# Optimization experiments

Hardware: AMD Instinct MI355X
Metric: run time of the kernel (lower is better)

## Reference

```python
import jax, jax.numpy as jnp
import numpy as np

N, E = 50000, 800000
IN_DIM, HID, OUT = 128, 64, 64
NEG_SLOPE = 0.2  # PyG GATConv default leaky_relu slope


def glorot(key, shape):
    fan_in, fan_out = shape[0], shape[-1]
    lim = jnp.sqrt(6.0 / (fan_in + fan_out))
    return jax.random.uniform(key, shape, minval=-lim, maxval=lim, dtype=jnp.float32)


def setup_inputs() -> dict:
    key = jax.random.key(0)
    ks = jax.random.split(key, 10)
    x = jax.random.normal(ks[0], (N, IN_DIM), dtype=jnp.float32)
    edge_index = jax.random.randint(ks[1], (2, E), 0, N, dtype=jnp.int64)
    # GATConv layer 1: heads=2, concat=False
    W1 = glorot(ks[2], (IN_DIM, 2 * HID))
    att_src1 = glorot(ks[3], (1, 2, HID))[0]   # [2, HID]
    att_dst1 = glorot(ks[4], (1, 2, HID))[0]
    b1 = jnp.zeros((HID,), jnp.float32)
    # GATConv layer 2: heads=1, concat=False
    W2 = glorot(ks[5], (HID, OUT))
    att_src2 = glorot(ks[6], (1, 1, OUT))[0]   # [1, OUT]
    att_dst2 = glorot(ks[7], (1, 1, OUT))[0]
    b2 = jnp.zeros((OUT,), jnp.float32)
    return {"x": x, "edge_index": edge_index, "W1": W1, "att_src1": att_src1,
            "att_dst1": att_dst1, "b1": b1, "W2": W2, "att_src2": att_src2,
            "att_dst2": att_dst2, "b2": b2}


def gat_conv(x, src, dst, W, att_src, att_dst, bias, heads, out_ch):
    n = x.shape[0]
    h = (x @ W).reshape(n, heads, out_ch)              # [N,H,C]
    a_src = jnp.einsum('nhc,hc->nh', h, att_src)       # [N,H]
    a_dst = jnp.einsum('nhc,hc->nh', h, att_dst)
    e = jax.nn.leaky_relu(a_src[src] + a_dst[dst], NEG_SLOPE)  # [E,H]
    # softmax over incoming edges per destination node (stable)
    e_max = jax.ops.segment_max(e, dst, num_segments=n)
    ex = jnp.exp(e - e_max[dst])
    denom = jax.ops.segment_sum(ex, dst, num_segments=n)
    alpha = ex / (denom[dst] + 1e-16)                  # [E,H]
    msg = h[src] * alpha[:, :, None]                   # [E,H,C]
    out = jax.ops.segment_sum(msg, dst, num_segments=n)
    return out.mean(axis=1) + bias                     # concat=False -> head mean


def reference(x, edge_index, W1, att_src1, att_dst1, b1, W2, att_src2, att_dst2, b2):
    n = x.shape[0]
    loop = jnp.arange(n, dtype=edge_index.dtype)
    src = jnp.concatenate([edge_index[0], loop])       # PyG add_self_loops
    dst = jnp.concatenate([edge_index[1], loop])
    x1 = gat_conv(x, src, dst, W1, att_src1, att_dst1, b1, 2, HID)
    x1 = jax.nn.elu(x1)
    # eval mode: dropedge and dropout are identity
    out = gat_conv(x1, src, dst, W2, att_src2, att_dst2, b2, 1, OUT)
    return out
```

## Files before the change

### kernel.cpp

```cpp
#include <hip/hip_runtime.h>
#include <math.h>

#define IN_DIM 128
#define HID 64
#define NEG_SLOPE 0.2f
#define CHUNK 4096
#define GCAP 6144

typedef __attribute__((ext_vector_type(8))) short bf16x8;
typedef __attribute__((ext_vector_type(4))) float f32x4;
typedef __attribute__((ext_vector_type(2))) float v2f;

__device__ __forceinline__ float wmax(float v){
  #pragma unroll
  for (int o = 32; o > 0; o >>= 1) v = fmaxf(v, __shfl_xor(v, o));
  return v;
}
__device__ __forceinline__ float wsum(float v){
  #pragma unroll
  for (int o = 32; o > 0; o >>= 1) v += __shfl_xor(v, o);
  return v;
}
__device__ __forceinline__ unsigned short f2bf(float f){
  union { float f; unsigned u; } v; v.f = f;
  unsigned r = v.u + 0x7fffu + ((v.u >> 16) & 1u);
  return (unsigned short)(r >> 16);
}
__device__ __forceinline__ float bl(unsigned u){
  union { unsigned u; float f; } v; v.u = u << 16; return v.f;
}
__device__ __forceinline__ float bh(unsigned u){
  union { unsigned u; float f; } v; v.u = u & 0xffff0000u; return v.f;
}
__device__ __forceinline__ v2f up2(unsigned u){
  v2f r; r[0] = bl(u); r[1] = bh(u); return r;
}

__device__ __forceinline__ void incl_scan256(int* sh, int tid){
  #pragma unroll
  for (int off = 1; off < 256; off <<= 1){
    int v = sh[tid];
    if (tid >= off) v += sh[tid - off];
    __syncthreads();
    sh[tid] = v;
    __syncthreads();
  }
}


__global__ __launch_bounds__(256) void prep(const int* __restrict__ ei, int E, int NBLK,
                                            unsigned* __restrict__ packed,
                                            int* __restrict__ binCnt,
                                            const float* __restrict__ W1,
                                            const float* __restrict__ W2,
                                            unsigned short* __restrict__ W1t,
                                            unsigned short* __restrict__ W2t,
                                            int* __restrict__ row_ptr, int N){
  int tid = threadIdx.x;
  if ((int)blockIdx.x < NBLK){
    __shared__ int lh[256];
    lh[tid] = 0; __syncthreads();
    int base = blockIdx.x * CHUNK;
    #pragma unroll
    for (int j = 0; j < CHUNK / 256; j++){
      int e = base + j * 256 + tid;
      if (e < E){
        unsigned s = (unsigned)ei[e];
        unsigned d = (unsigned)ei[E + e];
        packed[e] = (d << 16) | s;
        atomicAdd(&lh[d >> 8], 1);
      }
    }
    __syncthreads();
    if (lh[tid] > 0) atomicAdd(&binCnt[tid], lh[tid]);
  } else {
    int t = (blockIdx.x - NBLK) * 256 + tid;
    if (t < 128 * 128){
      int n = t >> 7, k = t & 127;
      W1t[n * 128 + k] = f2bf(W1[k * 128 + n]);
    }
    int t2 = t - 128 * 128;
    if (t2 >= 0 && t2 < 64 * 64){
      int n = t2 >> 6, k = t2 & 63;
      W2t[n * 64 + k] = f2bf(W2[k * 64 + n]);
    }
    if (t == 0) row_ptr[N] = E;
  }
}

__global__ __launch_bounds__(256) void scatter_bins(const unsigned* __restrict__ packed, int E,
                                                    const int* __restrict__ binCnt,
                                                    int* __restrict__ binOff,
                                                    unsigned* __restrict__ binned){
  __shared__ int bc[256], lh[256], lbase[256], gpos[256], lcur[256];
  __shared__ unsigned buf[CHUNK];
  int tid = threadIdx.x;
  int cg = binCnt[tid];
  bc[tid] = cg;
  lh[tid] = 0;
  __syncthreads();
  incl_scan256(bc, tid);
  int binBase_t = bc[tid] - cg;
  int base = blockIdx.x * CHUNK;
  int rem = E - base;
  unsigned v[CHUNK / 256];
  #pragma unroll
  for (int j = 0; j < CHUNK / 256; j++){
    int i = j * 256 + tid;
    if (i < rem){ v[j] = packed[base + i]; atomicAdd(&lh[v[j] >> 24], 1); }
  }
  __syncthreads();
  lbase[tid] = lh[tid]; __syncthreads();
  incl_scan256(lbase, tid);
  int myExcl = tid ? lbase[tid - 1] : 0;
  __syncthreads();
  lbase[tid] = myExcl;
  lcur[tid] = myExcl;
  if (lh[tid] > 0) gpos[tid] = binBase_t + atomicAdd(&binOff[tid], lh[tid]);
  __syncthreads();
  #pragma unroll
  for (int j = 0; j < CHUNK / 256; j++){
    int i = j * 256 + tid;
    if (i < rem){
      int b = v[j] >> 24;
      int p = atomicAdd(&lcur[b], 1);
      buf[p] = v[j];
    }
  }
  __syncthreads();
  int cn = rem < CHUNK ? rem : CHUNK;
  for (int i = tid; i < cn; i += 256){
    unsigned u = buf[i];
    int b = u >> 24;
    binned[gpos[b] + (i - lbase[b])] = u;
  }
}

__global__ __launch_bounds__(256) void group_sort(const unsigned* __restrict__ binned,
                                                  const int* __restrict__ binCnt,
                                                  unsigned* __restrict__ sorted,
                                                  int* __restrict__ row_ptr, int N){
  __shared__ unsigned A[GCAP], B[GCAP];
  __shared__ int sc[256], h2[256], rs[256], cur[256];
  int g = blockIdx.x, tid = threadIdx.x;
  int cg = binCnt[tid];
  sc[tid] = cg;
  h2[tid] = 0;
  __syncthreads();
  incl_scan256(sc, tid);
  int base = sc[g] - binCnt[g];
  int cnt = binCnt[g]; if (cnt > GCAP) cnt = GCAP;
  __syncthreads();
  for (int i = tid; i < cnt; i += 256){
    unsigned u = binned[base + i];
    A[i] = u;
    atomicAdd(&h2[(u >> 16) & 255], 1);
  }
  __syncthreads();
  rs[tid] = h2[tid]; __syncthreads();
  incl_scan256(rs, tid);
  int excl = tid ? rs[tid - 1] : 0;
  __syncthreads();
  rs[tid] = excl; cur[tid] = excl;
  int d = g * 256 + tid;
  if (d < N) row_ptr[d] = base + excl;
  __syncthreads();
  for (int i = tid; i < cnt; i += 256){
    unsigned u = A[i];
    int p = atomicAdd(&cur[(u >> 16) & 255], 1);
    B[p] = u;
  }
  __syncthreads();
  for (int i = tid; i < cnt; i += 256)
    sorted[base + i] = B[i];
}


template<int K, int NC, int HEADS>
__global__ __launch_bounds__(512) void gemm_mfma(const float* __restrict__ X,
    const unsigned short* __restrict__ Wt, const float* __restrict__ asrc,
    const float* __restrict__ adst, unsigned short* __restrict__ Hb,
    float* __restrict__ aa, int n_rows)
{
  constexpr int MT = 128;
  constexpr int KP = K + 8;
  constexpr int CP = NC + 4;
  constexpr int MF = MT / 16;
  constexpr int NFt = NC / 16;
  constexpr int WPN = 8 / NFt;
  constexpr int MFW = MF / WPN;
  constexpr unsigned SM1 = (unsigned)(MT + NC) * KP * 2;
  constexpr unsigned SM2 = (unsigned)MT * CP * 4;
  __shared__ char smem[SM1 > SM2 ? SM1 : SM2];
  unsigned short* xa = (unsigned short*)smem;
  unsigned short* wl = xa + MT * KP;
  int tid = threadIdx.x;
  int n0 = blockIdx.x * MT;

  for (int idx = tid; idx < MT * (K / 4); idx += 512){
    int n = idx / (K / 4), k4 = idx % (K / 4);
    float4 v = make_float4(0.f, 0.f, 0.f, 0.f);
    if (n0 + n < n_rows) v = *(const float4*)&X[(size_t)(n0 + n) * K + k4 * 4];
    ushort4 pk; pk.x = f2bf(v.x); pk.y = f2bf(v.y); pk.z = f2bf(v.z); pk.w = f2bf(v.w);
    *(ushort4*)&xa[n * KP + k4 * 4] = pk;
  }
  for (int idx = tid; idx < NC * (K / 8); idx += 512){
    int n = idx / (K / 8), k8 = idx % (K / 8);
    uint4 v = *(const uint4*)&Wt[(size_t)n * K + k8 * 8];
    *(uint4*)&wl[n * KP + k8 * 8] = v;
  }
  __syncthreads();

  int lane = tid & 63, w = tid >> 6;
  int m = lane & 15, q = lane >> 4;
  int nf = w % NFt;
  int mseg = w / NFt;
  f32x4 acc[MFW];
  #pragma unroll
  for (int i = 0; i < MFW; i++)
    #pragma unroll
    for (int r = 0; r < 4; r++) acc[i][r] = 0.f;

  #pragma unroll
  for (int ks = 0; ks < K / 32; ks++){
    bf16x8 bg = *(const bf16x8*)&wl[(nf * 16 + m) * KP + ks * 32 + q * 8];
    #pragma unroll
    for (int i = 0; i < MFW; i++){
      bf16x8 af = *(const bf16x8*)&xa[((mseg * MFW + i) * 16 + m) * KP + ks * 32 + q * 8];
      acc[i] = __builtin_amdgcn_mfma_f32_16x16x32_bf16(af, bg, acc[i], 0, 0, 0);
    }
  }
  __syncthreads();
  float* C = (float*)smem;
  #pragma unroll
  for (int i = 0; i < MFW; i++)
    #pragma unroll
    for (int r = 0; r < 4; r++)
      C[((mseg * MFW + i) * 16 + q * 4 + r) * CP + nf * 16 + m] = acc[i][r];
  __syncthreads();

  constexpr int CH = NC / 4;
  int row = tid >> 2;
  int c0 = (tid & 3) * CH;
  int n = n0 + row;
  int head = (HEADS == 2) ? (c0 >> 6) : 0;
  float s_p = 0.f, d_p = 0.f;
  unsigned short hb[CH];
  #pragma unroll
  for (int c = 0; c < CH; c += 4){
    f32x4 v = *(const f32x4*)&C[row * CP + c0 + c];
    #pragma unroll
    for (int u = 0; u < 4; u++){
      int ch = (c0 + c + u) & 63;
      s_p += v[u] * asrc[head * 64 + ch];
      d_p += v[u] * adst[head * 64 + ch];
      hb[c + u] = f2bf(v[u]);
    }
  }
  if (n < n_rows){
    #pragma unroll
    for (int c = 0; c < CH; c += 8){
      uint4 pk;
      pk.x = (unsigned)hb[c]     | ((unsigned)hb[c + 1] << 16);
      pk.y = (unsigned)hb[c + 2] | ((unsigned)hb[c + 3] << 16);
      pk.z = (unsigned)hb[c + 4] | ((unsigned)hb[c + 5] << 16);
      pk.w = (unsigned)hb[c + 6] | ((unsigned)hb[c + 7] << 16);
      *(uint4*)&Hb[(size_t)n * NC + c0 + c] = pk;
    }
  }
  s_p += __shfl_xor(s_p, 1);
  d_p += __shfl_xor(d_p, 1);
  if (HEADS == 2){
    if ((tid & 1) == 0 && n < n_rows){
      aa[(size_t)n * 4 + head]     = s_p;
      aa[(size_t)n * 4 + 2 + head] = d_p;
    }
  } else {
    s_p += __shfl_xor(s_p, 2);
    d_p += __shfl_xor(d_p, 2);
    if ((tid & 3) == 0 && n < n_rows){
      aa[(size_t)n * 2]     = s_p;
      aa[(size_t)n * 2 + 1] = d_p;
    }
  }
}


__global__ void agg_layer1(const int* __restrict__ row_ptr, const unsigned* __restrict__ sorted,
                           const float* __restrict__ aa, const unsigned short* __restrict__ h1b,
                           const float* __restrict__ b1, float* __restrict__ x1, int n_nodes){
  int d = (blockIdx.x * blockDim.x + threadIdx.x) >> 6;
  int lane = threadIdx.x & 63;
  if (d >= n_nodes) return;
  int rp0 = row_ptr[d];
  int deg = row_ptr[d + 1] - rp0;
  float2 adv = *(const float2*)&aa[d * 4 + 2];
  int s = -1;
  if (lane < deg) s = (int)(sorted[rp0 + lane] & 0xffffu);
  else if (lane == deg) s = d;
  float e0 = -INFINITY, e1 = -INFINITY;
  if (s >= 0){
    float2 asv = *(const float2*)&aa[s * 4];
    float t0 = asv.x + adv.x;
    float t1 = asv.y + adv.y;
    e0 = t0 >= 0.f ? t0 : NEG_SLOPE * t0;
    e1 = t1 >= 0.f ? t1 : NEG_SLOPE * t1;
  }
  float m0 = wmax(e0), m1 = wmax(e1);
  float p0 = (s >= 0) ? __expf(e0 - m0) : 0.f;
  float p1 = (s >= 0) ? __expf(e1 - m1) : 0.f;
  float al0 = p0 / (wsum(p0) + 1e-16f);
  float al1 = p1 / (wsum(p1) + 1e-16f);
  int ne = deg + 1;
  int g = lane >> 4, c = lane & 15;
  v2f acc[4] = {{0.f,0.f},{0.f,0.f},{0.f,0.f},{0.f,0.f}};
  #pragma unroll 2
  for (int j0 = 0; j0 < ne; j0 += 4){
    int j = j0 + g;
    int sj = __shfl(s, j);
    float a0 = __shfl(al0, j);
    float a1 = __shfl(al1, j);
    if (j < ne){
      uint4 v = ((const uint4*)(h1b + (size_t)sj * 128))[c];
      float a = (c < 8) ? a0 : a1;
      v2f av = {a, a};
      acc[0] = av * up2(v.x) + acc[0];
      acc[1] = av * up2(v.y) + acc[1];
      acc[2] = av * up2(v.z) + acc[2];
      acc[3] = av * up2(v.w) + acc[3];
    }
  }
  float accf[8] = {acc[0][0], acc[0][1], acc[1][0], acc[1][1],
                   acc[2][0], acc[2][1], acc[3][0], acc[3][1]};
  #pragma unroll
  for (int i = 0; i < 8; i++){
    accf[i] += __shfl_xor(accf[i], 16);
    accf[i] += __shfl_xor(accf[i], 32);
  }
  float outv[8];
  #pragma unroll
  for (int i = 0; i < 8; i++){
    float o = __shfl_xor(accf[i], 8);
    outv[i] = 0.5f * (accf[i] + o);
  }
  if (g == 0 && c < 8){
    float r[8];
    #pragma unroll
    for (int i = 0; i < 8; i++){
      float v = outv[i] + b1[c * 8 + i];
      r[i] = v > 0.f ? v : expm1f(v);
    }
    float* p = &x1[(size_t)d * 64 + c * 8];
    *(float4*)p       = make_float4(r[0], r[1], r[2], r[3]);
    *(float4*)(p + 4) = make_float4(r[4], r[5], r[6], r[7]);
  }
}

__global__ void agg_layer2(const int* __restrict__ row_ptr, const unsigned* __restrict__ sorted,
                           const float* __restrict__ aa, const unsigned short* __restrict__ h2b,
                           const float* __restrict__ b2, float* __restrict__ out, int n_nodes){
  int d = (blockIdx.x * blockDim.x + threadIdx.x) >> 6;
  int lane = threadIdx.x & 63;
  if (d >= n_nodes) return;
  int rp0 = row_ptr[d];
  int deg = row_ptr[d + 1] - rp0;
  float ad = aa[d * 2 + 1];
  int s = -1;
  if (lane < deg) s = (int)(sorted[rp0 + lane] & 0xffffu);
  else if (lane == deg) s = d;
  float e = -INFINITY;
  if (s >= 0){
    float t = aa[s * 2 + 0] + ad;
    e = t >= 0.f ? t : NEG_SLOPE * t;
  }
  float m = wmax(e);
  float p = (s >= 0) ? __expf(e - m) : 0.f;
  float al = p / (wsum(p) + 1e-16f);
  int ne = deg + 1;
  int g = lane >> 3, c = lane & 7;
  v2f acc[4] = {{0.f,0.f},{0.f,0.f},{0.f,0.f},{0.f,0.f}};
  #pragma unroll 2
  for (int j0 = 0; j0 < ne; j0 += 8){
    int j = j0 + g;
    int sj = __shfl(s, j);
    float a = __shfl(al, j);
    if (j < ne){
      uint4 v = ((const uint4*)(h2b + (size_t)sj * 64))[c];
      v2f av = {a, a};
      acc[0] = av * up2(v.x) + acc[0];
      acc[1] = av * up2(v.y) + acc[1];
      acc[2] = av * up2(v.z) + acc[2];
      acc[3] = av * up2(v.w) + acc[3];
    }
  }
  float accf[8] = {acc[0][0], acc[0][1], acc[1][0], acc[1][1],
                   acc[2][0], acc[2][1], acc[3][0], acc[3][1]};
  #pragma unroll
  for (int i = 0; i < 8; i++){
    accf[i] += __shfl_xor(accf[i], 8);
    accf[i] += __shfl_xor(accf[i], 16);
    accf[i] += __shfl_xor(accf[i], 32);
  }
  if (lane < 8){
    float r[8];
    #pragma unroll
    for (int i = 0; i < 8; i++) r[i] = accf[i] + b2[lane * 8 + i];
    float* q = &out[(size_t)d * 64 + lane * 8];
    *(float4*)q       = make_float4(r[0], r[1], r[2], r[3]);
    *(float4*)(q + 4) = make_float4(r[4], r[5], r[6], r[7]);
  }
}

extern "C" void kernel_launch(void* const* d_in, const int* in_sizes, int n_in,
                              void* d_out, int out_size, void* d_ws, size_t ws_size,
                              hipStream_t stream){
  const float* x     = (const float*)d_in[0];
  const int*   ei    = (const int*)d_in[1];
  const float* W1    = (const float*)d_in[2];
  const float* asrc1 = (const float*)d_in[3];
  const float* adst1 = (const float*)d_in[4];
  const float* b1    = (const float*)d_in[5];
  const float* W2    = (const float*)d_in[6];
  const float* asrc2 = (const float*)d_in[7];
  const float* adst2 = (const float*)d_in[8];
  const float* b2    = (const float*)d_in[9];
  float* out = (float*)d_out;
  int N = in_sizes[0] / IN_DIM;
  int E = in_sizes[1] / 2;
  int NG = (N + 255) >> 8;
  int NBLK = (E + CHUNK - 1) / CHUNK;
  int ngrp = (N + 3) / 4;

  char* p = (char*)d_ws;
  unsigned short* h1b = (unsigned short*)p;  p += (size_t)N * 128 * 2;
  unsigned short* h2b = (unsigned short*)p;  p += (size_t)N * 64 * 2;
  float* x1  = (float*)p;                    p += (size_t)N * 64 * 4;
  float* aa1 = (float*)p;                    p += (size_t)N * 4 * 4;
  float* aa2 = (float*)p;                    p += (size_t)N * 2 * 4;
  unsigned* packed = (unsigned*)p;           p += (size_t)E * 4;
  unsigned* binned = (unsigned*)p;           p += (size_t)E * 4;
  unsigned* sorted = (unsigned*)p;           p += (size_t)E * 4;
  int* row_ptr   = (int*)p;                  p += (size_t)(N + 1) * 4;
  int* binCnt    = (int*)p;                  p += 256 * 4;
  int* binOff    = (int*)p;                  p += 256 * 4;
  unsigned short* W1t = (unsigned short*)p;  p += 128 * 128 * 2;
  unsigned short* W2t = (unsigned short*)p;

  hipMemsetAsync(binCnt, 0, 512 * sizeof(int), stream);
  prep<<<NBLK + 80, 256, 0, stream>>>(ei, E, NBLK, packed, binCnt,
                                      W1, W2, W1t, W2t, row_ptr, N);
  scatter_bins<<<NBLK, 256, 0, stream>>>(packed, E, binCnt, binOff, binned);
  group_sort<<<NG, 256, 0, stream>>>(binned, binCnt, sorted, row_ptr, N);
  gemm_mfma<128, 128, 2><<<(N + 127) / 128, 512, 0, stream>>>(
      x, W1t, asrc1, adst1, h1b, aa1, N);
  agg_layer1<<<ngrp, 256, 0, stream>>>(row_ptr, sorted, aa1, h1b, b1, x1, N);
  gemm_mfma<64, 64, 1><<<(N + 127) / 128, 512, 0, stream>>>(
      x1, W2t, asrc2, adst2, h2b, aa2, N);
  agg_layer2<<<ngrp, 256, 0, stream>>>(row_ptr, sorted, aa2, h2b, b2, out, N);
}
```

Before: 235.9 us.

## Fuse layer-1 aggregation with layer-2 GEMM via per-block bf16 MFMA tile

Layer-1 aggregation and the layer-2 linear transform now run in one kernel. Each 64-thread block aggregates 16 destination nodes in sequence, writes the ELU outputs as bf16 into shared memory, then runs a 16x64x64 MFMA against W2t and writes h2b and the attention scalars directly. This removes the fp32 x1 round trip through global memory and one kernel launch. In exchange each wave handles its 16 nodes serially, block-level parallelism is lower, and x1 is now rounded to bf16 before the GEMM.

```diff
diff --git a/kernel.cpp b/kernel.cpp
--- a/kernel.cpp
+++ b/kernel.cpp
@@ -285,76 +285,137 @@
   }
 }
 
-
-__global__ void agg_layer1(const int* __restrict__ row_ptr, const unsigned* __restrict__ sorted,
-                           const float* __restrict__ aa, const unsigned short* __restrict__ h1b,
-                           const float* __restrict__ b1, float* __restrict__ x1, int n_nodes){
-  int d = (blockIdx.x * blockDim.x + threadIdx.x) >> 6;
-  int lane = threadIdx.x & 63;
-  if (d >= n_nodes) return;
-  int rp0 = row_ptr[d];
-  int deg = row_ptr[d + 1] - rp0;
-  float2 adv = *(const float2*)&aa[d * 4 + 2];
-  int s = -1;
-  if (lane < deg) s = (int)(sorted[rp0 + lane] & 0xffffu);
-  else if (lane == deg) s = d;
-  float e0 = -INFINITY, e1 = -INFINITY;
-  if (s >= 0){
-    float2 asv = *(const float2*)&aa[s * 4];
-    float t0 = asv.x + adv.x;
-    float t1 = asv.y + adv.y;
-    e0 = t0 >= 0.f ? t0 : NEG_SLOPE * t0;
-    e1 = t1 >= 0.f ? t1 : NEG_SLOPE * t1;
-  }
-  float m0 = wmax(e0), m1 = wmax(e1);
-  float p0 = (s >= 0) ? __expf(e0 - m0) : 0.f;
-  float p1 = (s >= 0) ? __expf(e1 - m1) : 0.f;
-  float al0 = p0 / (wsum(p0) + 1e-16f);
-  float al1 = p1 / (wsum(p1) + 1e-16f);
-  int ne = deg + 1;
+__global__ __launch_bounds__(64) void agg1_gemm2(const int* __restrict__ row_ptr,
+    const unsigned* __restrict__ sorted, const float* __restrict__ aa,
+    const unsigned short* __restrict__ h1b, const float* __restrict__ b1,
+    const unsigned short* __restrict__ W2t, const float* __restrict__ asrc2,
+    const float* __restrict__ adst2, unsigned short* __restrict__ h2b,
+    float* __restrict__ aa2, int n_nodes)
+{
+  __shared__ unsigned short xt[16 * 72];
+  __shared__ float Cl[16 * 68];
+  int lane = threadIdx.x;
+  int d0 = blockIdx.x * 16;
+
   int g = lane >> 4, c = lane & 15;
-  v2f acc[4] = {{0.f,0.f},{0.f,0.f},{0.f,0.f},{0.f,0.f}};
-  #pragma unroll 2
-  for (int j0 = 0; j0 < ne; j0 += 4){
-    int j = j0 + g;
-    int sj = __shfl(s, j);
-    float a0 = __shfl(al0, j);
-    float a1 = __shfl(al1, j);
-    if (j < ne){
-      uint4 v = ((const uint4*)(h1b + (size_t)sj * 128))[c];
-      float a = (c < 8) ? a0 : a1;
-      v2f av = {a, a};
-      acc[0] = av * up2(v.x) + acc[0];
-      acc[1] = av * up2(v.y) + acc[1];
-      acc[2] = av * up2(v.z) + acc[2];
-      acc[3] = av * up2(v.w) + acc[3];
-    }
-  }
-  float accf[8] = {acc[0][0], acc[0][1], acc[1][0], acc[1][1],
-                   acc[2][0], acc[2][1], acc[3][0], acc[3][1]};
-  #pragma unroll
-  for (int i = 0; i < 8; i++){
-    accf[i] += __shfl_xor(accf[i], 16);
-    accf[i] += __shfl_xor(accf[i], 32);
-  }
-  float outv[8];
-  #pragma unroll
-  for (int i = 0; i < 8; i++){
-    float o = __shfl_xor(accf[i], 8);
-    outv[i] = 0.5f * (accf[i] + o);
-  }
-  if (g == 0 && c < 8){
-    float r[8];
+  for (int jd = 0; jd < 16; jd++){
+    int d = d0 + jd;
+    if (d >= n_nodes) break;
+    int rp0 = row_ptr[d];
+    int deg = row_ptr[d + 1] - rp0;
+    float2 adv = *(const float2*)&aa[d * 4 + 2];
+    int s = -1;
+    if (lane < deg) s = (int)(sorted[rp0 + lane] & 0xffffu);
+    else if (lane == deg) s = d;
+    float e0 = -INFINITY, e1 = -INFINITY;
+    if (s >= 0){
+      float2 asv = *(const float2*)&aa[s * 4];
+      float t0 = asv.x + adv.x;
+      float t1 = asv.y + adv.y;
+      e0 = t0 >= 0.f ? t0 : NEG_SLOPE * t0;
+      e1 = t1 >= 0.f ? t1 : NEG_SLOPE * t1;
+    }
+    float m0 = wmax(e0), m1 = wmax(e1);
+    float p0 = (s >= 0) ? __expf(e0 - m0) : 0.f;
+    float p1 = (s >= 0) ? __expf(e1 - m1) : 0.f;
+    float al0 = p0 / (wsum(p0) + 1e-16f);
+    float al1 = p1 / (wsum(p1) + 1e-16f);
+    int ne = deg + 1;
+    v2f acc[4] = {{0.f,0.f},{0.f,0.f},{0.f,0.f},{0.f,0.f}};
+    #pragma unroll 2
+    for (int j0 = 0; j0 < ne; j0 += 4){
+      int j = j0 + g;
+      int sj = __shfl(s, j);
+      float a0 = __shfl(al0, j);
+      float a1 = __shfl(al1, j);
+      if (j < ne){
+        uint4 v = ((const uint4*)(h1b + (size_t)sj * 128))[c];
+        float a = (c < 8) ? a0 : a1;
+        v2f av = {a, a};
+        acc[0] = av * up2(v.x) + acc[0];
+        acc[1] = av * up2(v.y) + acc[1];
+        acc[2] = av * up2(v.z) + acc[2];
+        acc[3] = av * up2(v.w) + acc[3];
+      }
+    }
+    float accf[8] = {acc[0][0], acc[0][1], acc[1][0], acc[1][1],
+                     acc[2][0], acc[2][1], acc[3][0], acc[3][1]};
     #pragma unroll
     for (int i = 0; i < 8; i++){
-      float v = outv[i] + b1[c * 8 + i];
-      r[i] = v > 0.f ? v : expm1f(v);
-    }
-    float* p = &x1[(size_t)d * 64 + c * 8];
-    *(float4*)p       = make_float4(r[0], r[1], r[2], r[3]);
-    *(float4*)(p + 4) = make_float4(r[4], r[5], r[6], r[7]);
-  }
-}
+      accf[i] += __shfl_xor(accf[i], 16);
+      accf[i] += __shfl_xor(accf[i], 32);
+    }
+    float outv[8];
+    #pragma unroll
+    for (int i = 0; i < 8; i++){
+      float o = __shfl_xor(accf[i], 8);
+      outv[i] = 0.5f * (accf[i] + o);
+    }
+    if (g == 0 && c < 8){
+      unsigned short rb[8];
+      #pragma unroll
+      for (int i = 0; i < 8; i++){
+        float v = outv[i] + b1[c * 8 + i];
+        rb[i] = f2bf(v > 0.f ? v : expm1f(v));
+      }
+      uint4 pk;
+      pk.x = (unsigned)rb[0] | ((unsigned)rb[1] << 16);
+      pk.y = (unsigned)rb[2] | ((unsigned)rb[3] << 16);
+      pk.z = (unsigned)rb[4] | ((unsigned)rb[5] << 16);
+      pk.w = (unsigned)rb[6] | ((unsigned)rb[7] << 16);
+      *(uint4*)&xt[jd * 72 + c * 8] = pk;
+    }
+  }
+  __syncthreads();
+
+  int m = lane & 15, q = lane >> 4;
+  f32x4 cacc[4];
+  #pragma unroll
+  for (int nf = 0; nf < 4; nf++)
+    #pragma unroll
+    for (int r = 0; r < 4; r++) cacc[nf][r] = 0.f;
+  #pragma unroll
+  for (int ks = 0; ks < 2; ks++){
+    bf16x8 af = *(const bf16x8*)&xt[m * 72 + ks * 32 + q * 8];
+    #pragma unroll
+    for (int nf = 0; nf < 4; nf++){
+      bf16x8 bg = *(const bf16x8*)&W2t[(size_t)(nf * 16 + m) * 64 + ks * 32 + q * 8];
+      cacc[nf] = __builtin_amdgcn_mfma_f32_16x16x32_bf16(af, bg, cacc[nf], 0, 0, 0);
+    }
+  }
+  #pragma unroll
+  for (int nf = 0; nf < 4; nf++)
+    #pragma unroll
+    for (int r = 0; r < 4; r++)
+      Cl[(q * 4 + r) * 68 + nf * 16 + m] = cacc[nf][r];
+  __syncthreads();
+
+  int row = lane >> 2, qt = lane & 3;
+  int n = d0 + row;
+  float sp = 0.f, dp = 0.f;
+  unsigned pk[8];
+  #pragma unroll
+  for (int c2 = 0; c2 < 8; c2++){
+    int ch = qt * 16 + c2 * 2;
+    float v0 = Cl[row * 68 + ch];
+    float v1 = Cl[row * 68 + ch + 1];
+    sp += v0 * asrc2[ch] + v1 * asrc2[ch + 1];
+    dp += v0 * adst2[ch] + v1 * adst2[ch + 1];
+    pk[c2] = (unsigned)f2bf(v0) | ((unsigned)f2bf(v1) << 16);
+  }
+  if (n < n_nodes){
+    uint4* dst = (uint4*)&h2b[(size_t)n * 64 + qt * 16];
+    dst[0] = make_uint4(pk[0], pk[1], pk[2], pk[3]);
+    dst[1] = make_uint4(pk[4], pk[5], pk[6], pk[7]);
+  }
+  sp += __shfl_xor(sp, 1); dp += __shfl_xor(dp, 1);
+  sp += __shfl_xor(sp, 2); dp += __shfl_xor(dp, 2);
+  if (qt == 0 && n < n_nodes){
+    aa2[(size_t)n * 2]     = sp;
+    aa2[(size_t)n * 2 + 1] = dp;
+  }
+}
+
 
 __global__ void agg_layer2(const int* __restrict__ row_ptr, const unsigned* __restrict__ sorted,
                            const float* __restrict__ aa, const unsigned short* __restrict__ h2b,
@@ -434,7 +495,6 @@
   char* p = (char*)d_ws;
   unsigned short* h1b = (unsigned short*)p;  p += (size_t)N * 128 * 2;
   unsigned short* h2b = (unsigned short*)p;  p += (size_t)N * 64 * 2;
-  float* x1  = (float*)p;                    p += (size_t)N * 64 * 4;
   float* aa1 = (float*)p;                    p += (size_t)N * 4 * 4;
   float* aa2 = (float*)p;                    p += (size_t)N * 2 * 4;
   unsigned* packed = (unsigned*)p;           p += (size_t)E * 4;
@@ -453,8 +513,7 @@
   group_sort<<<NG, 256, 0, stream>>>(binned, binCnt, sorted, row_ptr, N);
   gemm_mfma<128, 128, 2><<<(N + 127) / 128, 512, 0, stream>>>(
       x, W1t, asrc1, adst1, h1b, aa1, N);
-  agg_layer1<<<ngrp, 256, 0, stream>>>(row_ptr, sorted, aa1, h1b, b1, x1, N);
-  gemm_mfma<64, 64, 1><<<(N + 127) / 128, 512, 0, stream>>>(
-      x1, W2t, asrc2, adst2, h2b, aa2, N);
+  agg1_gemm2<<<(N + 15) / 16, 64, 0, stream>>>(
+      row_ptr, sorted, aa1, h1b, b1, W2t, asrc2, adst2, h2b, aa2, N);
   agg_layer2<<<ngrp, 256, 0, stream>>>(row_ptr, sorted, aa2, h2b, b2, out, N);
 }
```

New measurement: 274.5 us. 1.16x slower.

## Co-schedule layer-1 GEMM tiles with edge-sort kernels via block-index dispatch

Applied to the files above, without the earlier changes.

Merges the scatter-bins and group-sort stages with halves of the layer-1 GEMM into two combined launches. Block index picks either a sort role or a 64-row MFMA GEMM tile role, and both share one 53 KB shared-memory union. The goal is to fill idle CUs during the latency-bound sort phases and save one launch. In exchange the GEMM tiles are smaller (64 rows, 256 threads) and every block reserves the largest shared footprint, which may reduce occupancy.

```diff
diff --git a/kernel.cpp b/kernel.cpp
--- a/kernel.cpp
+++ b/kernel.cpp
@@ -6,6 +6,7 @@
 #define NEG_SLOPE 0.2f
 #define CHUNK 4096
 #define GCAP 6144
+#define SMEM_UNION 53248
 
 typedef __attribute__((ext_vector_type(8))) short bf16x8;
 typedef __attribute__((ext_vector_type(4))) float f32x4;
@@ -44,6 +45,224 @@
     __syncthreads();
     sh[tid] = v;
     __syncthreads();
+  }
+}
+
+
+__device__ void scatter_body(char* smem, const unsigned* __restrict__ packed, int E,
+                             const int* __restrict__ binCnt, int* __restrict__ binOff,
+                             unsigned* __restrict__ binned, int bx){
+  int* ib = (int*)smem;
+  int* bc = ib;
+  int* lh = ib + 256;
+  int* lbase = ib + 512;
+  int* gpos = ib + 768;
+  int* lcur = ib + 1024;
+  unsigned* buf = (unsigned*)(ib + 1280);
+  int tid = threadIdx.x;
+  int cg = binCnt[tid];
+  bc[tid] = cg;
+  lh[tid] = 0;
+  __syncthreads();
+  incl_scan256(bc, tid);
+  int binBase_t = bc[tid] - cg;
+  int base = bx * CHUNK;
+  int rem = E - base;
+  unsigned v[CHUNK / 256];
+  #pragma unroll
+  for (int j = 0; j < CHUNK / 256; j++){
+    int i = j * 256 + tid;
+    if (i < rem){ v[j] = packed[base + i]; atomicAdd(&lh[v[j] >> 24], 1); }
+  }
+  __syncthreads();
+  lbase[tid] = lh[tid]; __syncthreads();
+  incl_scan256(lbase, tid);
+  int myExcl = tid ? lbase[tid - 1] : 0;
+  __syncthreads();
+  lbase[tid] = myExcl;
+  lcur[tid] = myExcl;
+  if (lh[tid] > 0) gpos[tid] = binBase_t + atomicAdd(&binOff[tid], lh[tid]);
+  __syncthreads();
+  #pragma unroll
+  for (int j = 0; j < CHUNK / 256; j++){
+    int i = j * 256 + tid;
+    if (i < rem){
+      int b = v[j] >> 24;
+      int p = atomicAdd(&lcur[b], 1);
+      buf[p] = v[j];
+    }
+  }
+  __syncthreads();
+  int cn = rem < CHUNK ? rem : CHUNK;
+  for (int i = tid; i < cn; i += 256){
+    unsigned u = buf[i];
+    int b = u >> 24;
+    binned[gpos[b] + (i - lbase[b])] = u;
+  }
+}
+
+__device__ void group_body(char* smem, const unsigned* __restrict__ binned,
+                           const int* __restrict__ binCnt, unsigned* __restrict__ sorted,
+                           int* __restrict__ row_ptr, int N, int g){
+  unsigned* A = (unsigned*)smem;
+  unsigned* B = A + GCAP;
+  int* ib = (int*)(B + GCAP);
+  int* sc = ib;
+  int* h2 = ib + 256;
+  int* rs = ib + 512;
+  int* cur = ib + 768;
+  int tid = threadIdx.x;
+  int cg = binCnt[tid];
+  sc[tid] = cg;
+  h2[tid] = 0;
+  __syncthreads();
+  incl_scan256(sc, tid);
+  int base = sc[g] - binCnt[g];
+  int cnt = binCnt[g]; if (cnt > GCAP) cnt = GCAP;
+  __syncthreads();
+  for (int i = tid; i < cnt; i += 256){
+    unsigned u = binned[base + i];
+    A[i] = u;
+    atomicAdd(&h2[(u >> 16) & 255], 1);
+  }
+  __syncthreads();
+  rs[tid] = h2[tid]; __syncthreads();
+  incl_scan256(rs, tid);
+  int excl = tid ? rs[tid - 1] : 0;
+  __syncthreads();
+  rs[tid] = excl; cur[tid] = excl;
+  int d = g * 256 + tid;
+  if (d < N) row_ptr[d] = base + excl;
+  __syncthreads();
+  for (int i = tid; i < cnt; i += 256){
+    unsigned u = A[i];
+    int p = atomicAdd(&cur[(u >> 16) & 255], 1);
+    B[p] = u;
+  }
+  __syncthreads();
+  for (int i = tid; i < cnt; i += 256)
+    sorted[base + i] = B[i];
+}
+
+__device__ void gemm1_body(char* smem, const float* __restrict__ X,
+                           const unsigned short* __restrict__ Wt,
+                           const float* __restrict__ asrc, const float* __restrict__ adst,
+                           unsigned short* __restrict__ Hb, float* __restrict__ aa,
+                           int n_rows, int n0){
+  const int KP = 136, CP = 132;
+  unsigned short* xa = (unsigned short*)smem;
+  unsigned short* wl = xa + 64 * KP;
+  int tid = threadIdx.x;
+  for (int idx = tid; idx < 64 * 32; idx += 256){
+    int n = idx >> 5, k4 = idx & 31;
+    float4 v = make_float4(0.f, 0.f, 0.f, 0.f);
+    if (n0 + n < n_rows) v = *(const float4*)&X[(size_t)(n0 + n) * 128 + k4 * 4];
+    ushort4 pk; pk.x = f2bf(v.x); pk.y = f2bf(v.y); pk.z = f2bf(v.z); pk.w = f2bf(v.w);
+    *(ushort4*)&xa[n * KP + k4 * 4] = pk;
+  }
+  for (int idx = tid; idx < 128 * 16; idx += 256){
+    int n = idx >> 4, k8 = idx & 15;
+    uint4 v = *(const uint4*)&Wt[(size_t)n * 128 + k8 * 8];
+    *(uint4*)&wl[n * KP + k8 * 8] = v;
+  }
+  __syncthreads();
+
+  int lane = tid & 63, w = tid >> 6;
+  int m = lane & 15, q = lane >> 4;
+  f32x4 acc[4][2];
+  #pragma unroll
+  for (int i = 0; i < 4; i++)
+    #pragma unroll
+    for (int j = 0; j < 2; j++)
+      #pragma unroll
+      for (int r = 0; r < 4; r++) acc[i][j][r] = 0.f;
+  #pragma unroll
+  for (int ks = 0; ks < 4; ks++){
+    bf16x8 bg[2];
+    #pragma unroll
+    for (int j = 0; j < 2; j++)
+      bg[j] = *(const bf16x8*)&wl[((2 * w + j) * 16 + m) * KP + ks * 32 + q * 8];
+    #pragma unroll
+    for (int i = 0; i < 4; i++){
+      bf16x8 af = *(const bf16x8*)&xa[(i * 16 + m) * KP + ks * 32 + q * 8];
+      #pragma unroll
+      for (int j = 0; j < 2; j++)
+        acc[i][j] = __builtin_amdgcn_mfma_f32_16x16x32_bf16(af, bg[j], acc[i][j], 0, 0, 0);
+    }
+  }
+  __syncthreads();
+  float* C = (float*)smem;
+  #pragma unroll
+  for (int i = 0; i < 4; i++)
+    #pragma unroll
+    for (int j = 0; j < 2; j++)
+      #pragma unroll
+      for (int r = 0; r < 4; r++)
+        C[(i * 16 + q * 4 + r) * CP + (2 * w + j) * 16 + m] = acc[i][j][r];
+  __syncthreads();
+
+  int row = tid >> 2;
+  int c0 = (tid & 3) * 32;
+  int n = n0 + row;
+  int head = (tid & 3) >> 1;
+  float s_p = 0.f, d_p = 0.f;
+  unsigned short hb[32];
+  #pragma unroll
+  for (int c = 0; c < 32; c += 4){
+    f32x4 v = *(const f32x4*)&C[row * CP + c0 + c];
+    #pragma unroll
+    for (int u = 0; u < 4; u++){
+      int ch = (c0 + c + u) & 63;
+      s_p += v[u] * asrc[head * 64 + ch];
+      d_p += v[u] * adst[head * 64 + ch];
+      hb[c + u] = f2bf(v[u]);
+    }
+  }
+  if (n < n_rows){
+    #pragma unroll
+    for (int c = 0; c < 32; c += 8){
+      uint4 pk;
+      pk.x = (unsigned)hb[c]     | ((unsigned)hb[c + 1] << 16);
+      pk.y = (unsigned)hb[c + 2] | ((unsigned)hb[c + 3] << 16);
+      pk.z = (unsigned)hb[c + 4] | ((unsigned)hb[c + 5] << 16);
+      pk.w = (unsigned)hb[c + 6] | ((unsigned)hb[c + 7] << 16);
+      *(uint4*)&Hb[(size_t)n * 128 + c0 + c] = pk;
+    }
+  }
+  s_p += __shfl_xor(s_p, 1);
+  d_p += __shfl_xor(d_p, 1);
+  if ((tid & 1) == 0 && n < n_rows){
+    aa[(size_t)n * 4 + head]     = s_p;
+    aa[(size_t)n * 4 + 2 + head] = d_p;
+  }
+}
+
+
+__global__ __launch_bounds__(256) void sort_gemm_a(const unsigned* __restrict__ packed, int E,
+    const int* __restrict__ binCnt, int* __restrict__ binOff, unsigned* __restrict__ binned,
+    int NS, const float* __restrict__ X, const unsigned short* __restrict__ W1t,
+    const float* __restrict__ asrc1, const float* __restrict__ adst1,
+    unsigned short* __restrict__ h1b, float* __restrict__ aa1, int n_rows){
+  __shared__ char smem[SMEM_UNION];
+  int bx = blockIdx.x;
+  if (bx < NS){
+    scatter_body(smem, packed, E, binCnt, binOff, binned, bx);
+  } else {
+    gemm1_body(smem, X, W1t, asrc1, adst1, h1b, aa1, n_rows, (bx - NS) * 64);
+  }
+}
+
+__global__ __launch_bounds__(256) void sort_gemm_b(const unsigned* __restrict__ binned,
+    const int* __restrict__ binCnt, unsigned* __restrict__ sorted, int* __restrict__ row_ptr,
+    int N, int NS, int gofs, const float* __restrict__ X, const unsigned short* __restrict__ W1t,
+    const float* __restrict__ asrc1, const float* __restrict__ adst1,
+    unsigned short* __restrict__ h1b, float* __restrict__ aa1, int n_rows){
+  __shared__ char smem[SMEM_UNION];
+  int bx = blockIdx.x;
+  if (bx < NS){
+    group_body(smem, binned, binCnt, sorted, row_ptr, N, bx);
+  } else {
+    gemm1_body(smem, X, W1t, asrc1, adst1, h1b, aa1, n_rows, (gofs + bx - NS) * 64);
   }
 }
 
@@ -86,93 +305,6 @@
     }
     if (t == 0) row_ptr[N] = E;
   }
-}
-
-__global__ __launch_bounds__(256) void scatter_bins(const unsigned* __restrict__ packed, int E,
-                                                    const int* __restrict__ binCnt,
-                                                    int* __restrict__ binOff,
-                                                    unsigned* __restrict__ binned){
-  __shared__ int bc[256], lh[256], lbase[256], gpos[256], lcur[256];
-  __shared__ unsigned buf[CHUNK];
-  int tid = threadIdx.x;
-  int cg = binCnt[tid];
-  bc[tid] = cg;
-  lh[tid] = 0;
-  __syncthreads();
-  incl_scan256(bc, tid);
-  int binBase_t = bc[tid] - cg;
-  int base = blockIdx.x * CHUNK;
-  int rem = E - base;
-  unsigned v[CHUNK / 256];
-  #pragma unroll
-  for (int j = 0; j < CHUNK / 256; j++){
-    int i = j * 256 + tid;
-    if (i < rem){ v[j] = packed[base + i]; atomicAdd(&lh[v[j] >> 24], 1); }
-  }
-  __syncthreads();
-  lbase[tid] = lh[tid]; __syncthreads();
-  incl_scan256(lbase, tid);
-  int myExcl = tid ? lbase[tid - 1] : 0;
-  __syncthreads();
-  lbase[tid] = myExcl;
-  lcur[tid] = myExcl;
-  if (lh[tid] > 0) gpos[tid] = binBase_t + atomicAdd(&binOff[tid], lh[tid]);
-  __syncthreads();
-  #pragma unroll
-  for (int j = 0; j < CHUNK / 256; j++){
-    int i = j * 256 + tid;
-    if (i < rem){
-      int b = v[j] >> 24;
-      int p = atomicAdd(&lcur[b], 1);
-      buf[p] = v[j];
-    }
-  }
-  __syncthreads();
-  int cn = rem < CHUNK ? rem : CHUNK;
-  for (int i = tid; i < cn; i += 256){
-    unsigned u = buf[i];
-    int b = u >> 24;
-    binned[gpos[b] + (i - lbase[b])] = u;
-  }
-}
-
-__global__ __launch_bounds__(256) void group_sort(const unsigned* __restrict__ binned,
-                                                  const int* __restrict__ binCnt,
-                                                  unsigned* __restrict__ sorted,
-                                                  int* __restrict__ row_ptr, int N){
-  __shared__ unsigned A[GCAP], B[GCAP];
-  __shared__ int sc[256], h2[256], rs[256], cur[256];
-  int g = blockIdx.x, tid = threadIdx.x;
-  int cg = binCnt[tid];
-  sc[tid] = cg;
-  h2[tid] = 0;
-  __syncthreads();
-  incl_scan256(sc, tid);
-  int base = sc[g] - binCnt[g];
-  int cnt = binCnt[g]; if (cnt > GCAP) cnt = GCAP;
-  __syncthreads();
-  for (int i = tid; i < cnt; i += 256){
-    unsigned u = binned[base + i];
-    A[i] = u;
-    atomicAdd(&h2[(u >> 16) & 255], 1);
-  }
-  __syncthreads();
-  rs[tid] = h2[tid]; __syncthreads();
-  incl_scan256(rs, tid);
-  int excl = tid ? rs[tid - 1] : 0;
-  __syncthreads();
-  rs[tid] = excl; cur[tid] = excl;
-  int d = g * 256 + tid;
-  if (d < N) row_ptr[d] = base + excl;
-  __syncthreads();
-  for (int i = tid; i < cnt; i += 256){
-    unsigned u = A[i];
-    int p = atomicAdd(&cur[(u >> 16) & 255], 1);
-    B[p] = u;
-  }
-  __syncthreads();
-  for (int i = tid; i < cnt; i += 256)
-    sorted[base + i] = B[i];
 }
 
 
@@ -430,6 +562,9 @@
   int NG = (N + 255) >> 8;
   int NBLK = (E + CHUNK - 1) / CHUNK;
   int ngrp = (N + 3) / 4;
+  int GT = (N + 63) / 64;
+  int GA = GT / 2;
+  int GB = GT - GA;
 
   char* p = (char*)d_ws;
   unsigned short* h1b = (unsigned short*)p;  p += (size_t)N * 128 * 2;
@@ -449,10 +584,10 @@
   hipMemsetAsync(binCnt, 0, 512 * sizeof(int), stream);
   prep<<<NBLK + 80, 256, 0, stream>>>(ei, E, NBLK, packed, binCnt,
                                       W1, W2, W1t, W2t, row_ptr, N);
-  scatter_bins<<<NBLK, 256, 0, stream>>>(packed, E, binCnt, binOff, binned);
-  group_sort<<<NG, 256, 0, stream>>>(binned, binCnt, sorted, row_ptr, N);
-  gemm_mfma<128, 128, 2><<<(N + 127) / 128, 512, 0, stream>>>(
-      x, W1t, asrc1, adst1, h1b, aa1, N);
+  sort_gemm_a<<<NBLK + GA, 256, 0, stream>>>(packed, E, binCnt, binOff, binned,
+                                             NBLK, x, W1t, asrc1, adst1, h1b, aa1, N);
+  sort_gemm_b<<<NG + GB, 256, 0, stream>>>(binned, binCnt, sorted, row_ptr, N,
+                                           NG, GA, x, W1t, asrc1, adst1, h1b, aa1, N);
   agg_layer1<<<ngrp, 256, 0, stream>>>(row_ptr, sorted, aa1, h1b, b1, x1, N);
   gemm_mfma<64, 64, 1><<<(N + 127) / 128, 512, 0, stream>>>(
       x1, W2t, asrc2, adst2, h2b, aa2, N);
```

After: 235.6 us. No clear change (-0.1%).
